# Optimization experiments

Hardware: AMD Instinct MI355X
Metric: run time of the kernel (lower is better)

## Reference

```python
import jax, jax.numpy as jnp
import numpy as np

DIM = 2048
N_HEADS = 32
N_KV_HEADS = 8
HEAD_DIM = 64
BATCH = 2
SEQ = 2048
N_REP = N_HEADS // N_KV_HEADS
SCALE = HEAD_DIM ** -0.5
ROPE_BASE = 10000.0


def setup_inputs() -> dict:
    key = jax.random.key(0)
    ks = jax.random.split(key, 5)
    x = jax.random.normal(ks[0], (BATCH, SEQ, DIM), dtype=jnp.float32)
    # weights stored as (in, out) so projection is x @ W
    Wq = jax.random.normal(ks[1], (DIM, N_HEADS * HEAD_DIM), dtype=jnp.float32) * (DIM ** -0.5)
    Wk = jax.random.normal(ks[2], (DIM, N_KV_HEADS * HEAD_DIM), dtype=jnp.float32) * (DIM ** -0.5)
    Wv = jax.random.normal(ks[3], (DIM, N_KV_HEADS * HEAD_DIM), dtype=jnp.float32) * (DIM ** -0.5)
    Wo = jax.random.normal(ks[4], (N_HEADS * HEAD_DIM, DIM), dtype=jnp.float32) * ((N_HEADS * HEAD_DIM) ** -0.5)
    # RoPE tables (seq, head_dim)
    inv_freq = 1.0 / (ROPE_BASE ** (jnp.arange(0, HEAD_DIM, 2, dtype=jnp.float32) / HEAD_DIM))
    t = jnp.arange(SEQ, dtype=jnp.float32)
    freqs = jnp.outer(t, inv_freq)                      # (S, D/2)
    emb = jnp.concatenate([freqs, freqs], axis=-1)      # (S, D)
    cos = jnp.cos(emb)
    sin = jnp.sin(emb)
    # additive causal mask (1,1,S,S)
    neg = jnp.finfo(jnp.float32).min
    causal = jnp.tril(jnp.ones((SEQ, SEQ), dtype=bool))
    attention_mask = jnp.where(causal, 0.0, neg)[None, None, :, :].astype(jnp.float32)
    return {"x": x, "Wq": Wq, "Wk": Wk, "Wv": Wv, "Wo": Wo,
            "cos": cos, "sin": sin, "attention_mask": attention_mask}


def _rotate_half(u):
    h = u.shape[-1] // 2
    return jnp.concatenate([-u[..., h:], u[..., :h]], axis=-1)


def reference(x, Wq, Wk, Wv, Wo, cos, sin, attention_mask):
    b, s, _ = x.shape
    q = (x @ Wq).reshape(b, s, N_HEADS, HEAD_DIM)
    k = (x @ Wk).reshape(b, s, N_KV_HEADS, HEAD_DIM)
    v = (x @ Wv).reshape(b, s, N_KV_HEADS, HEAD_DIM)
    # RoPE, broadcast over head dim (unsqueeze_dim=2)
    c = cos[None, :, None, :]
    sn = sin[None, :, None, :]
    q = q * c + _rotate_half(q) * sn
    k = k * c + _rotate_half(k) * sn
    # repeat KV heads for GQA: (b,s,kvh,d) -> (b,s,h,d)
    k = jnp.repeat(k, N_REP, axis=2)
    v = jnp.repeat(v, N_REP, axis=2)
    # (b,h,s,d)
    q = q.transpose(0, 2, 1, 3)
    k = k.transpose(0, 2, 1, 3)
    v = v.transpose(0, 2, 1, 3)
    scores = jnp.einsum("bhqd,bhkd->bhqk", q, k) * SCALE + attention_mask
    attn = jax.nn.softmax(scores.astype(jnp.float32), axis=-1).astype(q.dtype)
    out = jnp.einsum("bhqk,bhkd->bhqd", attn, v)
    out = out.transpose(0, 2, 1, 3).reshape(b, s, N_HEADS * HEAD_DIM)
    return out @ Wo
```

## Files before the change

kernel.cpp:

```cpp
#include <hip/hip_runtime.h>
#include <hip/hip_bf16.h>

typedef unsigned short u16;
typedef unsigned int   u32;
typedef __bf16 bf16_t;
typedef bf16_t bf16x8 __attribute__((ext_vector_type(8)));
typedef u16    u16x8  __attribute__((ext_vector_type(8)));
typedef float  f32x4  __attribute__((ext_vector_type(4)));

#define DIM  2048
#define SEQ  2048
#define BATCH 2
#define NH   32
#define NKVH 8
#define HD   64
#define KVDIM (NKVH*HD)
#define NQKV (DIM + 2*KVDIM)
#define SCALE 0.125f

__device__ __forceinline__ float b2f(u16 u) {
  union { u32 i; float f; } v; v.i = ((u32)u) << 16; return v.f;
}
__device__ __forceinline__ u16 f2b(float f) {
  union { float f; u32 i; } v; v.f = f;
  u32 x = v.i;
  return (u16)((x + 0x7fffu + ((x >> 16) & 1u)) >> 16);
}
__device__ __forceinline__ u32 pkbf2(float a, float b) {
  __hip_bfloat162 h = __float22bfloat162_rn(float2{a, b});
  union { __hip_bfloat162 h; u32 u; } v; v.h = h; return v.u;
}
__device__ __forceinline__ int probe_bf16(const u32* probe) { return probe[0] != 0u; }
__device__ __forceinline__ float ext_ld(const void* p, long idx, int mode_bf16) {
  return mode_bf16 ? b2f(((const u16*)p)[idx]) : ((const float*)p)[idx];
}
__device__ __forceinline__ void gload_lds16(const u16* g, u16* l) {
  __builtin_amdgcn_global_load_lds((const __attribute__((address_space(1))) void*)g,
                                   (__attribute__((address_space(3))) void*)l, 16, 0, 0);
}

__global__ void cast_x(const void* __restrict__ in, u16* __restrict__ out,
                       const u32* __restrict__ probe) {
  int mode = probe_bf16(probe);
  if (mode) return;
  long base = ((long)blockIdx.x * 256 + threadIdx.x) * 8;
  float4 f0 = *(const float4*)((const float*)in + base);
  float4 f1 = *(const float4*)((const float*)in + base + 4);
  u16x8 t;
  t[0] = f2b(f0.x); t[1] = f2b(f0.y); t[2] = f2b(f0.z); t[3] = f2b(f0.w);
  t[4] = f2b(f1.x); t[5] = f2b(f1.y); t[6] = f2b(f1.z); t[7] = f2b(f1.w);
  *(u16x8*)&out[base] = t;
}

__global__ void transpose_qkv(const void* __restrict__ Wq, const void* __restrict__ Wk,
                              const void* __restrict__ Wv, u16* __restrict__ out,
                              const u32* __restrict__ probe) {
  int mode = probe_bf16(probe);
  __shared__ u16 t[32][33];
  int xt = blockIdx.x;
  const void* in; int C, c0, obase;
  if (xt < 64)      { in = Wq; C = DIM;   c0 = xt * 32;        obase = 0; }
  else if (xt < 80) { in = Wk; C = KVDIM; c0 = (xt - 64) * 32; obase = DIM; }
  else              { in = Wv; C = KVDIM; c0 = (xt - 80) * 32; obase = DIM + KVDIM; }
  int r0 = blockIdx.y * 32;
  int tx = threadIdx.x, ty = threadIdx.y;
#pragma unroll
  for (int i = 0; i < 32; i += 8)
    t[ty + i][tx] = mode ? ((const u16*)in)[(long)(r0 + ty + i) * C + c0 + tx]
                         : f2b(((const float*)in)[(long)(r0 + ty + i) * C + c0 + tx]);
  __syncthreads();
#pragma unroll
  for (int i = 0; i < 32; i += 8)
    out[(long)(obase + c0 + ty + i) * DIM + r0 + tx] = t[tx][ty + i];
}

__global__ void transpose_w(const void* __restrict__ in, u16* __restrict__ out,
                            int R, int C, const u32* __restrict__ probe) {
  int mode = probe_bf16(probe);
  __shared__ u16 t[32][33];
  int c0 = blockIdx.x * 32, r0 = blockIdx.y * 32;
  int tx = threadIdx.x, ty = threadIdx.y;
#pragma unroll
  for (int i = 0; i < 32; i += 8)
    t[ty + i][tx] = mode ? ((const u16*)in)[(long)(r0 + ty + i) * C + c0 + tx]
                         : f2b(((const float*)in)[(long)(r0 + ty + i) * C + c0 + tx]);
  __syncthreads();
#pragma unroll
  for (int i = 0; i < 32; i += 8)
    out[(long)(c0 + ty + i) * R + r0 + tx] = t[tx][ty + i];
}

__global__ void rope_both(u16* __restrict__ Qb, u16* __restrict__ Kb,
                          const void* __restrict__ cosb, const void* __restrict__ sinb,
                          const u32* __restrict__ probe) {
  int mode = probe_bf16(probe);
  long gid = (long)blockIdx.x * 256 + threadIdx.x;
  const long NQp = (long)BATCH * SEQ * NH * 32;
  u16* base_p; int n_heads; long t; float osc;
  if (gid < NQp) { base_p = Qb; n_heads = NH; t = gid; osc = SCALE; }
  else           { base_p = Kb; n_heads = NKVH; t = gid - NQp; osc = 1.0f; }
  int pair = t & 31;
  long t2 = t >> 5;
  int h = (int)(t2 % n_heads);
  long row = t2 / n_heads;
  int s = (int)(row & (SEQ - 1));
  long base = row * (n_heads * HD) + h * HD + pair;
  float q0 = b2f(base_p[base]), q1 = b2f(base_p[base + 32]);
  float c0 = ext_ld(cosb, (long)s * HD + pair, mode);
  float c1 = ext_ld(cosb, (long)s * HD + pair + 32, mode);
  float s0 = ext_ld(sinb, (long)s * HD + pair, mode);
  float s1 = ext_ld(sinb, (long)s * HD + pair + 32, mode);
  base_p[base]      = f2b((q0 * c0 - q1 * s0) * osc);
  base_p[base + 32] = f2b((q1 * c1 + q0 * s1) * osc);
}


#define WAITV(N) asm volatile("s_waitcnt vmcnt(%0)" :: "n"(N) : "memory")
#define WAITL()  asm volatile("s_waitcnt lgkmcnt(0)" ::: "memory")
#define BARR()   __builtin_amdgcn_s_barrier()
#define SCHEDB() __builtin_amdgcn_sched_barrier(0)
#define PRIO1()  __builtin_amdgcn_s_setprio(1)
#define PRIO0()  __builtin_amdgcn_s_setprio(0)

#define STAGE_A(h, bufi, kt) do { _Pragma("unroll") \
  for (int _j = 0; _j < AL; ++_j) \
    gload_lds16(Ax + aSrcOff[h][_j] + (kt) * 64, (u16*)&As[(bufi) * (BM * 64) + aDst[h][_j]]); } while (0)

#define STAGE_B(h, bufi, kt) do { _Pragma("unroll") \
  for (int _j = 0; _j < 2; ++_j) \
    gload_lds16(Bt + bSrcOff[h][_j] + (kt) * 64, (u16*)&Bs[(bufi) * (256 * 64) + bDst[h][_j]]); } while (0)

#define LDA_HALF(Lp, mh) do { _Pragma("unroll") \
  for (int _m = 0; _m < MH2; ++_m) { \
    const u16* _r = (Lp) + (wm * WM + (mh) * (WM / 2) + _m * 16 + l16) * 64; \
    af[_m][0] = *(const bf16x8*)&_r[sw0]; \
    af[_m][1] = *(const bf16x8*)&_r[sw1]; } } while (0)

#define LDB_HALF(Lp, nh) do { _Pragma("unroll") \
  for (int _n = 0; _n < 2; ++_n) { \
    const u16* _r = (Lp) + (wn * 64 + (nh) * 32 + _n * 16 + l16) * 64; \
    bfr[nh][_n][0] = *(const bf16x8*)&_r[sw0]; \
    bfr[nh][_n][1] = *(const bf16x8*)&_r[sw1]; } } while (0)

#define MFMA_Q(mh, nh) do { _Pragma("unroll") \
  for (int _m = 0; _m < MH2; ++_m) \
    _Pragma("unroll") \
    for (int _n = 0; _n < 2; ++_n) { \
      f32x4 _z = acc[(mh) * MH2 + _m][(nh) * 2 + _n]; \
      _z = __builtin_amdgcn_mfma_f32_16x16x32_bf16(af[_m][0], bfr[nh][_n][0], _z, 0, 0, 0); \
      _z = __builtin_amdgcn_mfma_f32_16x16x32_bf16(af[_m][1], bfr[nh][_n][1], _z, 0, 0, 0); \
      acc[(mh) * MH2 + _m][(nh) * 2 + _n] = _z; } } while (0)

template<int BM, int EPI>
__device__ __forceinline__ void gemm8_core(const u16* __restrict__ Ax, const u16* __restrict__ Bt,
                                           u16* __restrict__ Qb, u16* __restrict__ Kb,
                                           u16* __restrict__ Vt, void* __restrict__ Cout,
                                           const u32* __restrict__ probe) {
  constexpr int WM  = BM / 2;
  constexpr int MI  = WM / 16;
  constexpr int MH2 = MI / 2;
  constexpr int AL  = BM / 128;
  constexpr int VM_A = 6 + 3 * AL;
  constexpr int VM_B = 4 + 4 * AL;
  constexpr int K = DIM;
  __shared__ __align__(16) u16 As[2 * BM * 64];
  __shared__ __align__(16) u16 Bs[2 * 256 * 64];

  int tid = threadIdx.x, lane = tid & 63, wv = tid >> 6;
  int l16 = lane & 15, q = lane >> 4;
  int wm = wv >> 2, wn = wv & 3;
  int bm0 = blockIdx.y * BM, bn0 = blockIdx.x * 256;

  int srow = lane >> 3;
  int scolb = ((lane & 7) ^ srow) * 8;
  int e7 = l16 & 7;
  int sw0 = (q ^ e7) * 8, sw1 = ((4 + q) ^ e7) * 8;

  int aSrcOff[2][AL], aDst[2][AL];
#pragma unroll
  for (int h = 0; h < 2; ++h)
#pragma unroll
    for (int j = 0; j < AL; ++j) {
      int g = wv * AL + j;
      int rb = (BM == 256) ? ((g >> 3) * 128 + h * 64 + (g & 7) * 8)
                           : ((g >> 2) * 64 + h * 32 + (g & 3) * 8);
      aSrcOff[h][j] = (bm0 + rb + srow) * K + scolb;
      aDst[h][j] = rb * 64 + lane * 8;
    }
  int bSrcOff[2][2], bDst[2][2];
#pragma unroll
  for (int h = 0; h < 2; ++h)
#pragma unroll
    for (int j = 0; j < 2; ++j) {
      int g = wv * 2 + j;
      int rb = (g >> 2) * 64 + h * 32 + (g & 3) * 8;
      bSrcOff[h][j] = (bn0 + rb + srow) * K + scolb;
      bDst[h][j] = rb * 64 + lane * 8;
    }

  const u16* As0 = As;  const u16* As1 = As + BM * 64;
  const u16* Bs0 = Bs;  const u16* Bs1 = Bs + 256 * 64;

  f32x4 acc[MI][4] = {};
  bf16x8 af[MH2][2];
  bf16x8 bfr[2][2][2];

  STAGE_A(0, 0, 0);
  STAGE_B(0, 0, 0);
  STAGE_B(1, 0, 0);
  STAGE_A(1, 0, 0);
  STAGE_A(0, 1, 1);
  STAGE_B(0, 1, 1);
  STAGE_B(1, 1, 1);

#pragma unroll 1
  for (int i = 0; i < 16; ++i) {
    int te = 2 * i + 2; if (te > 31) te = 31;
    int to = 2 * i + 3; if (to > 31) to = 31;
    SCHEDB();
    STAGE_A(1, 1, 2 * i + 1);
    WAITV(VM_A); BARR(); SCHEDB();
    LDA_HALF(As0, 0); LDB_HALF(Bs0, 0);
    WAITL(); BARR();
    PRIO1(); MFMA_Q(0, 0); PRIO0();
    SCHEDB();
    STAGE_A(0, 0, te);
    WAITV(VM_B); BARR(); SCHEDB();
    LDB_HALF(Bs0, 1);
    WAITL(); BARR();
    PRIO1(); MFMA_Q(0, 1); PRIO0();
    SCHEDB();
    STAGE_B(0, 0, te);
    WAITV(VM_A); BARR(); SCHEDB();
    LDA_HALF(As0, 1);
    WAITL(); BARR();
    PRIO1(); MFMA_Q(1, 0); PRIO0();
    SCHEDB();
    STAGE_B(1, 0, te);
    PRIO1(); MFMA_Q(1, 1); PRIO0();
    SCHEDB();
    STAGE_A(1, 0, te);
    WAITV(VM_A); BARR(); SCHEDB();
    LDA_HALF(As1, 0); LDB_HALF(Bs1, 0);
    WAITL(); BARR();
    PRIO1(); MFMA_Q(0, 0); PRIO0();
    SCHEDB();
    STAGE_A(0, 1, to);
    WAITV(VM_B); BARR(); SCHEDB();
    LDB_HALF(Bs1, 1);
    WAITL(); BARR();
    PRIO1(); MFMA_Q(0, 1); PRIO0();
    SCHEDB();
    STAGE_B(0, 1, to);
    WAITV(VM_A); BARR(); SCHEDB();
    LDA_HALF(As1, 1);
    WAITL(); BARR();
    PRIO1(); MFMA_Q(1, 0); PRIO0();
    SCHEDB();
    STAGE_B(1, 1, to);
    PRIO1(); MFMA_Q(1, 1); PRIO0();
  }

  if constexpr (EPI == 0) {
    if (bn0 < DIM) {
#pragma unroll
      for (int mi = 0; mi < MI; ++mi)
#pragma unroll
        for (int ni = 0; ni < 4; ++ni)
#pragma unroll
          for (int r = 0; r < 4; ++r) {
            int m = bm0 + wm * WM + mi * 16 + q * 4 + r;
            int n = bn0 + wn * 64 + ni * 16 + l16;
            Qb[(long)m * DIM + n] = f2b(acc[mi][ni][r]);
          }
    } else if (bn0 < DIM + KVDIM) {
#pragma unroll
      for (int mi = 0; mi < MI; ++mi)
#pragma unroll
        for (int ni = 0; ni < 4; ++ni)
#pragma unroll
          for (int r = 0; r < 4; ++r) {
            int m = bm0 + wm * WM + mi * 16 + q * 4 + r;
            int n = bn0 - DIM + wn * 64 + ni * 16 + l16;
            Kb[(long)m * KVDIM + n] = f2b(acc[mi][ni][r]);
          }
    } else {
#pragma unroll
      for (int mi = 0; mi < MI; ++mi)
#pragma unroll
        for (int ni = 0; ni < 4; ++ni) {
          int vcol = bn0 - (DIM + KVDIM) + wn * 64 + ni * 16 + l16;
          int kvh2 = vcol >> 6, d = vcol & 63;
          int m0 = bm0 + wm * WM + mi * 16 + q * 4;
          int bb = m0 >> 11, s = m0 & (SEQ - 1);
          uint2 w;
          w.x = pkbf2(acc[mi][ni][0], acc[mi][ni][1]);
          w.y = pkbf2(acc[mi][ni][2], acc[mi][ni][3]);
          *(uint2*)&Vt[((long)(bb * NKVH + kvh2) * HD + d) * SEQ + s] = w;
        }
    }
  } else {
    int mode = probe_bf16(probe);
#pragma unroll
    for (int mi = 0; mi < MI; ++mi)
#pragma unroll
      for (int ni = 0; ni < 4; ++ni)
#pragma unroll
        for (int r = 0; r < 4; ++r) {
          int m = bm0 + wm * WM + mi * 16 + q * 4 + r;
          int n = bn0 + wn * 64 + ni * 16 + l16;
          long idx = (long)m * DIM + n;
          if (mode) ((u16*)Cout)[idx] = f2b(acc[mi][ni][r]);
          else      ((float*)Cout)[idx] = acc[mi][ni][r];
        }
  }
}

__global__ __launch_bounds__(512, 2)
void gemm_qkv8(const void* __restrict__ x, const u16* __restrict__ xb,
               const u16* __restrict__ Bt, u16* __restrict__ Qb, u16* __restrict__ Kb,
               u16* __restrict__ Vt, const u32* __restrict__ probe) {
  const u16* Ax = probe_bf16(probe) ? (const u16*)x : xb;
  gemm8_core<256, 0>(Ax, Bt, Qb, Kb, Vt, nullptr, probe);
}

__global__ __launch_bounds__(512, 2)
void gemm_ao8(const u16* __restrict__ A, const u16* __restrict__ Bt,
              void* __restrict__ C, const u32* __restrict__ probe) {
  gemm8_core<128, 1>(A, Bt, nullptr, nullptr, nullptr, C, probe);
}

__launch_bounds__(256)
__global__ void gemm_qkv(const void* __restrict__ A, const u16* __restrict__ Bt,
                         u16* __restrict__ Qb, u16* __restrict__ Kb, u16* __restrict__ Vt,
                         int a_half, const u32* __restrict__ probe) {
  int mode = a_half || probe_bf16(probe);
  __shared__ __align__(16) u16 As[128 * 32];
  __shared__ __align__(16) u16 Bs[128 * 32];
  int tid = threadIdx.x, lane = tid & 63, wv = tid >> 6;
  int l16 = lane & 15, q = lane >> 4;
  int bm0 = blockIdx.y * 128, bn0 = blockIdx.x * 128;
  int mbase = (wv & 1) * 64, nbase = (wv >> 1) * 64;
  int c0 = tid, c1 = tid + 256;
  int r0 = c0 >> 2, s0 = (c0 & 3) ^ ((r0 >> 1) & 3);
  int r1 = c1 >> 2, s1 = (c1 & 3) ^ ((r1 >> 1) & 3);
  const int K = DIM;
  long aoff0 = (long)(bm0 + r0) * K + s0 * 8;
  long aoff1 = (long)(bm0 + r1) * K + s1 * 8;
  long boff0 = (long)(bn0 + r0) * K + s0 * 8;
  long boff1 = (long)(bn0 + r1) * K + s1 * 8;
  int rsw = (q ^ ((l16 >> 1) & 3)) * 8;
  f32x4 acc[4][4] = {};
  for (int k0 = 0; k0 < K; k0 += 32) {
    __syncthreads();
    if (mode) {
      gload_lds16((const u16*)A + aoff0 + k0, &As[wv * 512]);
      gload_lds16((const u16*)A + aoff1 + k0, &As[2048 + wv * 512]);
    } else {
      const float* Af = (const float*)A;
      float4 f0 = *(const float4*)(Af + aoff0 + k0);
      float4 f1 = *(const float4*)(Af + aoff0 + k0 + 4);
      u16x8 t;
      t[0] = f2b(f0.x); t[1] = f2b(f0.y); t[2] = f2b(f0.z); t[3] = f2b(f0.w);
      t[4] = f2b(f1.x); t[5] = f2b(f1.y); t[6] = f2b(f1.z); t[7] = f2b(f1.w);
      *(u16x8*)&As[c0 * 8] = t;
      float4 g0 = *(const float4*)(Af + aoff1 + k0);
      float4 g1 = *(const float4*)(Af + aoff1 + k0 + 4);
      u16x8 u;
      u[0] = f2b(g0.x); u[1] = f2b(g0.y); u[2] = f2b(g0.z); u[3] = f2b(g0.w);
      u[4] = f2b(g1.x); u[5] = f2b(g1.y); u[6] = f2b(g1.z); u[7] = f2b(g1.w);
      *(u16x8*)&As[c1 * 8] = u;
    }
    gload_lds16(Bt + boff0 + k0, &Bs[wv * 512]);
    gload_lds16(Bt + boff1 + k0, &Bs[2048 + wv * 512]);
    __syncthreads();
    bf16x8 af[4], bfr[4];
#pragma unroll
    for (int mi = 0; mi < 4; mi++)
      af[mi] = *(const bf16x8*)&As[(mbase + mi * 16 + l16) * 32 + rsw];
#pragma unroll
    for (int ni = 0; ni < 4; ni++)
      bfr[ni] = *(const bf16x8*)&Bs[(nbase + ni * 16 + l16) * 32 + rsw];
#pragma unroll
    for (int mi = 0; mi < 4; mi++)
#pragma unroll
      for (int ni = 0; ni < 4; ni++)
        acc[mi][ni] = __builtin_amdgcn_mfma_f32_16x16x32_bf16(
            af[mi], bfr[ni], acc[mi][ni], 0, 0, 0);
  }
  if (bn0 < DIM + KVDIM) {
    u16* Cb; int ldc, ncol0;
    if (bn0 < DIM) { Cb = Qb; ldc = DIM; ncol0 = bn0; }
    else           { Cb = Kb; ldc = KVDIM; ncol0 = bn0 - DIM; }
#pragma unroll
    for (int mi = 0; mi < 4; mi++)
#pragma unroll
      for (int ni = 0; ni < 4; ni++)
#pragma unroll
        for (int r = 0; r < 4; r++) {
          int m = bm0 + mbase + mi * 16 + q * 4 + r;
          int n = ncol0 + nbase + ni * 16 + l16;
          Cb[(long)m * ldc + n] = f2b(acc[mi][ni][r]);
        }
  } else {
    int vcol0 = bn0 - DIM - KVDIM;
#pragma unroll
    for (int mi = 0; mi < 4; mi++)
#pragma unroll
      for (int ni = 0; ni < 4; ni++) {
        int vcol = vcol0 + nbase + ni * 16 + l16;
        int kvh2 = vcol >> 6, d = vcol & 63;
        int m = bm0 + mbase + mi * 16 + q * 4;
        int bb = m >> 11, s = m & (SEQ - 1);
        uint2 w;
        w.x = pkbf2(acc[mi][ni][0], acc[mi][ni][1]);
        w.y = pkbf2(acc[mi][ni][2], acc[mi][ni][3]);
        *(uint2*)&Vt[((long)(bb * NKVH + kvh2) * HD + d) * SEQ + s] = w;
      }
  }
}

__launch_bounds__(256, 4)
__global__ void attn_kernel(const u16* __restrict__ Q, const u16* __restrict__ K,
                            const u16* __restrict__ Vt, u16* __restrict__ AO) {
  __shared__ __align__(16) u16 Ks[64 * 64];
  __shared__ __align__(16) u16 Vs[64 * 64];
  __shared__ __align__(16) u16 Ps[4][16 * 64];
  int tid = threadIdx.x, lane = tid & 63, wv = tid >> 6;
  int l16 = lane & 15, q = lane >> 4;
  int i = blockIdx.x;
  int bh = blockIdx.y;
  int b = bh >> 5, h = bh & 31, kvh = h >> 2;
  const u16* Kp = K + (long)b * SEQ * KVDIM + kvh * HD;
  const u16* Vp = Vt + (long)(b * NKVH + kvh) * HD * SEQ;

  int cA = tid, cB = tid + 256;
  int rA = cA >> 3, bA = (cA & 7) ^ (rA & 7);
  int rB = cB >> 3, bB = (cB & 7) ^ (rB & 7);
  const u16* kSrcA = Kp + (long)rA * KVDIM + bA * 8;
  const u16* kSrcB = Kp + (long)rB * KVDIM + bB * 8;
  const u16* vSrcA = Vp + (long)rA * SEQ + bA * 8;
  const u16* vSrcB = Vp + (long)rB * SEQ + bB * 8;
  u16* kDstA = &Ks[(wv * 64 + lane) * 8];
  u16* kDstB = &Ks[(256 + wv * 64 + lane) * 8];
  u16* vDstA = &Vs[(wv * 64 + lane) * 8];
  u16* vDstB = &Vs[(256 + wv * 64 + lane) * 8];

  int e = l16 & 7;
  int off0 = (q ^ e) * 8;
  int off1 = ((4 + q) ^ e) * 8;

  bf16x8 ones;
#pragma unroll
  for (int j = 0; j < 8; j++) ones[j] = (bf16_t)1.0f;

#pragma unroll
  for (int ph = 0; ph < 2; ph++) {
    int t = ph ? (31 - i) : i;
    int qbase = t * 64 + wv * 16;
    const u16* Qp = Q + (long)(b * SEQ + qbase) * DIM + h * HD;
    bf16x8 aq0 = *(const bf16x8*)&Qp[l16 * DIM + q * 8];
    bf16x8 aq1 = *(const bf16x8*)&Qp[l16 * DIM + 32 + q * 8];
    f32x4 o_acc[4] = {};
    f32x4 l_acc = {};
    int qrow = qbase + l16;

    for (int kt = 0; kt <= t; kt++) {
      long kk = (long)kt * 64;
      __syncthreads();
      gload_lds16(kSrcA + kk * KVDIM, kDstA);
      gload_lds16(kSrcB + kk * KVDIM, kDstB);
      gload_lds16(vSrcA + kk, vDstA);
      gload_lds16(vSrcB + kk, vDstB);
      __syncthreads();

      f32x4 sc[4];
#pragma unroll
      for (int ni = 0; ni < 4; ni++) {
        bf16x8 bk0 = *(const bf16x8*)&Ks[(ni * 16 + l16) * 64 + off0];
        bf16x8 bk1 = *(const bf16x8*)&Ks[(ni * 16 + l16) * 64 + off1];
        f32x4 z = {};
        z = __builtin_amdgcn_mfma_f32_16x16x32_bf16(bk0, aq0, z, 0, 0, 0);
        z = __builtin_amdgcn_mfma_f32_16x16x32_bf16(bk1, aq1, z, 0, 0, 0);
        sc[ni] = z;
      }
      if (kt == t) {
#pragma unroll
        for (int ni = 0; ni < 4; ni++)
#pragma unroll
          for (int r = 0; r < 4; r++) {
            int kv = (int)kk + ni * 16 + q * 4 + r;
            float p = __expf(sc[ni][r]);
            sc[ni][r] = (kv <= qrow) ? p : 0.f;
          }
      } else {
#pragma unroll
        for (int ni = 0; ni < 4; ni++)
#pragma unroll
          for (int r = 0; r < 4; r++) sc[ni][r] = __expf(sc[ni][r]);
      }
#pragma unroll
      for (int ni = 0; ni < 4; ni++) {
        uint2 w;
        w.x = pkbf2(sc[ni][0], sc[ni][1]);
        w.y = pkbf2(sc[ni][2], sc[ni][3]);
        int pblk = (2 * ni + (q >> 1)) ^ e;
        *(uint2*)&Ps[wv][l16 * 64 + pblk * 8 + (q & 1) * 4] = w;
      }
      bf16x8 ap0 = *(const bf16x8*)&Ps[wv][l16 * 64 + off0];
      bf16x8 ap1 = *(const bf16x8*)&Ps[wv][l16 * 64 + off1];
      l_acc = __builtin_amdgcn_mfma_f32_16x16x32_bf16(ap0, ones, l_acc, 0, 0, 0);
      l_acc = __builtin_amdgcn_mfma_f32_16x16x32_bf16(ap1, ones, l_acc, 0, 0, 0);
#pragma unroll
      for (int di = 0; di < 4; di++) {
        bf16x8 bv0 = *(const bf16x8*)&Vs[(di * 16 + l16) * 64 + off0];
        bf16x8 bv1 = *(const bf16x8*)&Vs[(di * 16 + l16) * 64 + off1];
        o_acc[di] = __builtin_amdgcn_mfma_f32_16x16x32_bf16(ap0, bv0, o_acc[di], 0, 0, 0);
        o_acc[di] = __builtin_amdgcn_mfma_f32_16x16x32_bf16(ap1, bv1, o_acc[di], 0, 0, 0);
      }
    }
    long obase = (long)(b * SEQ + qbase + q * 4) * DIM + h * HD;
#pragma unroll
    for (int r = 0; r < 4; r++) {
      float inv = 1.0f / l_acc[r];
#pragma unroll
      for (int di = 0; di < 4; di++)
        AO[obase + (long)r * DIM + di * 16 + l16] = f2b(o_acc[di][r] * inv);
    }
  }
}

extern "C" void kernel_launch(void* const* d_in, const int* in_sizes, int n_in,
                              void* d_out, int out_size, void* d_ws, size_t ws_size,
                              hipStream_t stream) {
  const void* x    = d_in[0];
  const void* Wq   = d_in[1];
  const void* Wk   = d_in[2];
  const void* Wv   = d_in[3];
  const void* Wo   = d_in[4];
  const void* cosb = d_in[5];
  const void* sinb = d_in[6];
  const u32*  probe = (const u32*)d_in[7];

  u16* WqkvT = (u16*)d_ws;
  u16* WoT = WqkvT + (size_t)NQKV * DIM;
  u16* Qb  = WoT + (size_t)DIM * DIM;
  u16* Kb  = Qb  + (size_t)BATCH * SEQ * DIM;
  u16* Vt  = Kb  + (size_t)BATCH * SEQ * KVDIM;
  u16* xb  = Vt  + (size_t)BATCH * NKVH * HD * SEQ;
  u16* AO  = Qb;

  size_t need_xb = ((size_t)(xb - WqkvT) + (size_t)BATCH * SEQ * DIM) * sizeof(u16);
  int use_xb = ws_size >= need_xb;

  dim3 blk32(32, 8);
  transpose_qkv<<<dim3(96, 64), blk32, 0, stream>>>(Wq, Wk, Wv, WqkvT, probe);
  transpose_w<<<dim3(DIM / 32, DIM / 32), blk32, 0, stream>>>(Wo, WoT, DIM, DIM, probe);

  int M = BATCH * SEQ;
  if (use_xb) {
    cast_x<<<(M * DIM) / (256 * 8), 256, 0, stream>>>(x, xb, probe);
    gemm_qkv8<<<dim3(NQKV / 256, M / 256), 512, 0, stream>>>(x, xb, WqkvT, Qb, Kb, Vt, probe);
  } else {
    gemm_qkv<<<dim3(NQKV / 128, M / 128), 256, 0, stream>>>(x, WqkvT, Qb, Kb, Vt, 0, probe);
  }

  long rope_slots = (long)M * NH * 32 + (long)M * NKVH * 32;
  rope_both<<<(int)(rope_slots / 256), 256, 0, stream>>>(Qb, Kb, cosb, sinb, probe);

  attn_kernel<<<dim3(16, BATCH * NH), 256, 0, stream>>>(Qb, Kb, Vt, AO);

  gemm_ao8<<<dim3(DIM / 256, M / 128), 512, 0, stream>>>(AO, WoT, d_out, probe);
}
```

Measured before the change: 343.8 us.

## Restructure GEMM main loop into per-buffer vmcnt waits with interleaved LDS reads

Reworks the 8-wave GEMM pipeline so global-to-LDS stages are issued right after the LDS fragment reads of each quarter. Global-memory waits now happen only once per buffer half instead of before every quarter. Scheduling barriers are removed and barriers are placed around the MFMA blocks, the aim being to cut vmcnt stalls and let memory traffic overlap more of the matrix math. The risk is that LDS buffer reuse becomes racy if the single wait count is wrong for either tile size, and the compiler may reorder code now that it is unconstrained.

Measured after the change: 340.9 us. About the same (-0.8%).

```diff
diff --git a/kernel.cpp b/kernel.cpp
--- a/kernel.cpp
+++ b/kernel.cpp
@@ -118,7 +118,6 @@
 #define WAITV(N) asm volatile("s_waitcnt vmcnt(%0)" :: "n"(N) : "memory")
 #define WAITL()  asm volatile("s_waitcnt lgkmcnt(0)" ::: "memory")
 #define BARR()   __builtin_amdgcn_s_barrier()
-#define SCHEDB() __builtin_amdgcn_sched_barrier(0)
 #define PRIO1()  __builtin_amdgcn_s_setprio(1)
 #define PRIO0()  __builtin_amdgcn_s_setprio(0)
 
@@ -150,6 +149,8 @@
       _z = __builtin_amdgcn_mfma_f32_16x16x32_bf16(af[_m][0], bfr[nh][_n][0], _z, 0, 0, 0); \
       _z = __builtin_amdgcn_mfma_f32_16x16x32_bf16(af[_m][1], bfr[nh][_n][1], _z, 0, 0, 0); \
       acc[(mh) * MH2 + _m][(nh) * 2 + _n] = _z; } } while (0)
+
+#define VMS() do { if constexpr (BM == 256) WAITV(6); else WAITV(5); } while (0)
 
 template<int BM, int EPI>
 __device__ __forceinline__ void gemm8_core(const u16* __restrict__ Ax, const u16* __restrict__ Bt,
@@ -160,8 +161,6 @@
   constexpr int MI  = WM / 16;
   constexpr int MH2 = MI / 2;
   constexpr int AL  = BM / 128;
-  constexpr int VM_A = 6 + 3 * AL;
-  constexpr int VM_B = 4 + 4 * AL;
   constexpr int K = DIM;
   __shared__ __align__(16) u16 As[2 * BM * 64];
   __shared__ __align__(16) u16 Bs[2 * 256 * 64];
@@ -212,54 +211,45 @@
   STAGE_A(0, 1, 1);
   STAGE_B(0, 1, 1);
   STAGE_B(1, 1, 1);
+  VMS(); BARR();
 
 #pragma unroll 1
   for (int i = 0; i < 16; ++i) {
+    int t1 = 2 * i + 1;
     int te = 2 * i + 2; if (te > 31) te = 31;
     int to = 2 * i + 3; if (to > 31) to = 31;
-    SCHEDB();
-    STAGE_A(1, 1, 2 * i + 1);
-    WAITV(VM_A); BARR(); SCHEDB();
     LDA_HALF(As0, 0); LDB_HALF(Bs0, 0);
-    WAITL(); BARR();
-    PRIO1(); MFMA_Q(0, 0); PRIO0();
-    SCHEDB();
+    STAGE_A(1, 1, t1);
+    BARR(); WAITL();
+    PRIO1(); MFMA_Q(0, 0); PRIO0(); BARR();
+    LDB_HALF(Bs0, 1);
     STAGE_A(0, 0, te);
-    WAITV(VM_B); BARR(); SCHEDB();
-    LDB_HALF(Bs0, 1);
-    WAITL(); BARR();
-    PRIO1(); MFMA_Q(0, 1); PRIO0();
-    SCHEDB();
+    BARR(); WAITL();
+    PRIO1(); MFMA_Q(0, 1); PRIO0(); BARR();
+    LDA_HALF(As0, 1);
     STAGE_B(0, 0, te);
-    WAITV(VM_A); BARR(); SCHEDB();
-    LDA_HALF(As0, 1);
-    WAITL(); BARR();
-    PRIO1(); MFMA_Q(1, 0); PRIO0();
-    SCHEDB();
+    BARR(); WAITL();
+    PRIO1(); MFMA_Q(1, 0); PRIO0(); BARR();
     STAGE_B(1, 0, te);
+    VMS(); BARR();
     PRIO1(); MFMA_Q(1, 1); PRIO0();
-    SCHEDB();
+    LDA_HALF(As1, 0); LDB_HALF(Bs1, 0);
     STAGE_A(1, 0, te);
-    WAITV(VM_A); BARR(); SCHEDB();
-    LDA_HALF(As1, 0); LDB_HALF(Bs1, 0);
-    WAITL(); BARR();
-    PRIO1(); MFMA_Q(0, 0); PRIO0();
-    SCHEDB();
+    BARR(); WAITL();
+    PRIO1(); MFMA_Q(0, 0); PRIO0(); BARR();
+    LDB_HALF(Bs1, 1);
     STAGE_A(0, 1, to);
-    WAITV(VM_B); BARR(); SCHEDB();
-    LDB_HALF(Bs1, 1);
-    WAITL(); BARR();
-    PRIO1(); MFMA_Q(0, 1); PRIO0();
-    SCHEDB();
+    BARR(); WAITL();
+    PRIO1(); MFMA_Q(0, 1); PRIO0(); BARR();
+    LDA_HALF(As1, 1);
     STAGE_B(0, 1, to);
-    WAITV(VM_A); BARR(); SCHEDB();
-    LDA_HALF(As1, 1);
-    WAITL(); BARR();
-    PRIO1(); MFMA_Q(1, 0); PRIO0();
-    SCHEDB();
+    BARR(); WAITL();
+    PRIO1(); MFMA_Q(1, 0); PRIO0(); BARR();
     STAGE_B(1, 1, to);
+    VMS(); BARR();
     PRIO1(); MFMA_Q(1, 1); PRIO0();
   }
+  WAITV(0);
 
   if constexpr (EPI == 0) {
     if (bn0 < DIM) {
```
